# Kernel optimization log

Hardware: AMD Instinct MI355X
Metric: run time of the kernel (lower is better)

Reference implementation:

```python
import jax, jax.numpy as jnp
import numpy as np

B, S, E = 2, 2048, 1024
H, KV, D = 16, 4, 64
GC = 128          # ve_gate_channels
EPS = 1.1920929e-07  # torch F.rms_norm default eps for fp32
NEG = -1e30


def setup_inputs() -> dict:
    key = jax.random.key(0)
    ks = jax.random.split(key, 8)
    x = jax.random.normal(ks[0], (B, S, E), jnp.float32)
    ve = jax.random.normal(ks[1], (B, S, KV * D), jnp.float32)
    half = D // 2
    inv_freq = 1.0 / (10000.0 ** (np.arange(half, dtype=np.float64) / half))
    ang = np.arange(S, dtype=np.float64)[:, None] * inv_freq[None, :]
    cos = jnp.asarray(np.cos(ang), jnp.float32)[:, None, :]  # [S,1,D/2]
    sin = jnp.asarray(np.sin(ang), jnp.float32)[:, None, :]
    sc = E ** -0.5
    Wq = jax.random.normal(ks[2], (E, H * D), jnp.float32) * sc
    Wk = jax.random.normal(ks[3], (E, KV * D), jnp.float32) * sc
    Wv = jax.random.normal(ks[4], (E, KV * D), jnp.float32) * sc
    Wproj = jax.random.normal(ks[5], (E, E), jnp.float32) * sc
    Wgate = jax.random.normal(ks[6], (GC, KV), jnp.float32) * (GC ** -0.5)
    return {"x": x, "ve": ve, "cos": cos, "sin": sin, "Wq": Wq, "Wk": Wk,
            "Wv": Wv, "Wproj": Wproj, "Wgate": Wgate,
            "window_left": 1024, "window_right": 0}


def _rms(x):
    return x * jax.lax.rsqrt(jnp.mean(x * x, axis=-1, keepdims=True) + EPS)


def _rope(x, cos, sin):
    d = x.shape[-1] // 2
    x1, x2 = x[..., :d], x[..., d:]
    return jnp.concatenate([x1 * cos + x2 * sin, -x1 * sin + x2 * cos], axis=-1)


def reference(x, ve, cos, sin, Wq, Wk, Wv, Wproj, Wgate, window_left, window_right):
    b, s, e = x.shape
    q = (x @ Wq).reshape(b, s, H, D)
    k = (x @ Wk).reshape(b, s, KV, D)
    v = (x @ Wv).reshape(b, s, KV, D)
    # value-embedding gate: 2*sigmoid over first GC channels, per kv-head
    gate = 2.0 * jax.nn.sigmoid(x[..., :GC] @ Wgate)          # [B,S,KV]
    v = v + gate[..., None] * ve.reshape(b, s, KV, D)
    q = _rms(_rope(q, cos, sin))
    k = _rms(_rope(k, cos, sin))
    # GQA: repeat kv heads to match query heads
    g = H // KV
    kk = jnp.repeat(k, g, axis=2)                             # [B,S,H,D]
    vv = jnp.repeat(v, g, axis=2)
    scores = jnp.einsum('bihd,bjhd->bhij', q, kk) * (D ** -0.5)
    i = jnp.arange(s)[:, None]
    j = jnp.arange(s)[None, :]
    mask = (j <= i + window_right) & (j >= i - window_left) & (j <= i)
    scores = jnp.where(mask, scores, NEG)
    p = jax.nn.softmax(scores, axis=-1)
    y = jnp.einsum('bhij,bjhd->bihd', p, vv).reshape(b, s, H * D)
    return y @ Wproj
```

## Files before the change

kernel.cpp:

```cpp
#include <hip/hip_runtime.h>

typedef __bf16 bf16;
typedef __bf16 bf16x4 __attribute__((ext_vector_type(4)));
typedef __bf16 bf16x8 __attribute__((ext_vector_type(8)));
typedef float floatx4 __attribute__((ext_vector_type(4)));

#define EPS 1.1920929e-07f
#define QSCALE (0.125f * 1.44269504088896f)
#define SHIFT_C 11.5416f

__device__ __forceinline__ floatx4 mfma16(bf16x8 a, bf16x8 b, floatx4 c) {
  return __builtin_amdgcn_mfma_f32_16x16x32_bf16(a, b, c, 0, 0, 0);
}

__device__ __forceinline__ void gload16(const void* g, void* l) {
  __builtin_amdgcn_global_load_lds((const __attribute__((address_space(1))) unsigned int*)g,
                                   (__attribute__((address_space(3))) unsigned int*)l, 16, 0, 0);
}

__global__ void prep_kernel(const float* __restrict__ x, const float* __restrict__ wgate,
                            const float* __restrict__ Wq, const float* __restrict__ Wk,
                            const float* __restrict__ Wv, const float* __restrict__ Wproj,
                            bf16* __restrict__ xb, float* __restrict__ gate,
                            bf16* __restrict__ out_qkv, bf16* __restrict__ out_proj) {
  __shared__ float tile[32][33];
  const int tid = threadIdx.x;
  if (blockIdx.x < 4096) {
    int t = blockIdx.x;
    const float* xr = x + (size_t)t * 1024;
    float4 v = *(const float4*)(xr + tid * 4);
    bf16x4 o = {(bf16)v.x, (bf16)v.y, (bf16)v.z, (bf16)v.w};
    *(bf16x4*)(xb + (size_t)t * 1024 + tid * 4) = o;
    if (tid < 64) {
      int c = (tid & 31) * 4;
#pragma unroll
      for (int kv = 0; kv < 4; kv++) {
        float g = v.x * wgate[(c + 0) * 4 + kv] + v.y * wgate[(c + 1) * 4 + kv] +
                  v.z * wgate[(c + 2) * 4 + kv] + v.w * wgate[(c + 3) * 4 + kv];
        g += __shfl_xor(g, 1, 64);
        g += __shfl_xor(g, 2, 64);
        g += __shfl_xor(g, 4, 64);
        g += __shfl_xor(g, 8, 64);
        g += __shfl_xor(g, 16, 64);
        if (tid == 0) {
          int b = t >> 11, s = t & 2047;
          gate[((size_t)b * 4 + kv) * 2048 + s] = 2.f / (1.f + __expf(-g));
        }
      }
    }
  } else {
    int j = blockIdx.x - 4096;
    int ky = j / 80;
    int nx = j - ky * 80;
    int k0 = ky * 32;
    int tx = tid & 31, ty = tid >> 5;
    if (nx < 48) {
      int n0 = nx * 32;
#pragma unroll
      for (int i = 0; i < 4; i++) {
        int k = k0 + ty + i * 8, n = n0 + tx;
        float v;
        if (n < 1024)      v = Wq[(size_t)k * 1024 + n];
        else if (n < 1280) v = Wk[(size_t)k * 256 + (n - 1024)];
        else               v = Wv[(size_t)k * 256 + (n - 1280)];
        tile[ty + i * 8][tx] = v;
      }
      __syncthreads();
#pragma unroll
      for (int i = 0; i < 4; i++) {
        int n = n0 + ty + i * 8, k = k0 + tx;
        out_qkv[(size_t)n * 1024 + k] = (bf16)tile[tx][ty + i * 8];
      }
    } else {
      int n0 = (nx - 48) * 32;
#pragma unroll
      for (int i = 0; i < 4; i++)
        tile[ty + i * 8][tx] = Wproj[(size_t)(k0 + ty + i * 8) * 1024 + n0 + tx];
      __syncthreads();
#pragma unroll
      for (int i = 0; i < 4; i++)
        out_proj[(size_t)(n0 + ty + i * 8) * 1024 + k0 + tx] = (bf16)tile[tx][ty + i * 8];
    }
  }
}

__global__ __launch_bounds__(256) void qkv_gemm_kernel(const bf16* __restrict__ A,
                                                       const bf16* __restrict__ Bt,
                                                       const float* __restrict__ ve,
                                                       const float* __restrict__ cosb,
                                                       const float* __restrict__ sinb,
                                                       const float* __restrict__ gate,
                                                       bf16* __restrict__ Qb,
                                                       bf16* __restrict__ Kf,
                                                       bf16* __restrict__ Vf) {
  __shared__ __align__(16) char smem[24576];
  bf16* As = (bf16*)smem;
  bf16* Bs = (bf16*)(smem + 16384);
  bf16* Ep = (bf16*)smem;
  const int K = 1024;
  const int tid = threadIdx.x;
  const int orig = blockIdx.x;
  const int lid = (orig & 7) * 96 + (orig >> 3);
  const int tile = lid % 24;
  const int m0 = (lid / 24) * 128, n0 = tile * 64;
  const int w = tid >> 6, lane = tid & 63;
  const int q = lane >> 4, r0 = lane & 15;
  const int lrow = lane >> 2, lcol = (lane & 3) * 8;
  const int b = m0 >> 11, s0 = m0 & 2047;

  floatx4 acc[2][4];
#pragma unroll
  for (int i = 0; i < 2; i++)
#pragma unroll
    for (int j = 0; j < 4; j++) acc[i][j] = (floatx4){0.f, 0.f, 0.f, 0.f};

  for (int k0 = 0; k0 < K; k0 += 64) {
    __syncthreads();
#pragma unroll
    for (int i = 0; i < 4; i++) {
      int g = w * 4 + i, s = g >> 3, rb = g & 7;
      gload16(A + (size_t)(m0 + rb * 16 + lrow) * K + k0 + s * 32 + lcol, &As[s * 4096 + rb * 512]);
    }
#pragma unroll
    for (int i = 0; i < 2; i++) {
      int g = w * 2 + i, s = g >> 2, rb = g & 3;
      gload16(Bt + (size_t)(n0 + rb * 16 + lrow) * K + k0 + s * 32 + lcol, &Bs[s * 2048 + rb * 512]);
    }
    __syncthreads();
#pragma unroll
    for (int s = 0; s < 2; s++) {
      bf16x8 af[2], bfr[4];
#pragma unroll
      for (int mt = 0; mt < 2; mt++) af[mt] = *(const bf16x8*)&As[s * 4096 + (w * 32 + mt * 16 + r0) * 32 + q * 8];
#pragma unroll
      for (int nt = 0; nt < 4; nt++) bfr[nt] = *(const bf16x8*)&Bs[s * 2048 + (nt * 16 + r0) * 32 + q * 8];
#pragma unroll
      for (int mt = 0; mt < 2; mt++)
#pragma unroll
        for (int nt = 0; nt < 4; nt++)
          acc[mt][nt] = mfma16(af[mt], bfr[nt], acc[mt][nt]);
    }
  }
  __syncthreads();

  if (tile < 16) {
    const int h = tile;
#pragma unroll
    for (int mt = 0; mt < 2; mt++) {
      float rvv[4][4];
#pragma unroll
      for (int ntp = 0; ntp < 2; ntp++) {
        int d31 = ntp * 16 + r0;
#pragma unroll
        for (int r = 0; r < 4; r++) {
          int s = s0 + w * 32 + mt * 16 + q * 4 + r;
          float c = cosb[s * 32 + d31], sn = sinb[s * 32 + d31];
          float v1 = acc[mt][ntp][r], v2 = acc[mt][ntp + 2][r];
          rvv[ntp][r] = v1 * c + v2 * sn;
          rvv[ntp + 2][r] = v2 * c - v1 * sn;
        }
      }
#pragma unroll
      for (int r = 0; r < 4; r++) {
        float ss = 0.f;
#pragma unroll
        for (int nt = 0; nt < 4; nt++) ss += rvv[nt][r] * rvv[nt][r];
        ss += __shfl_xor(ss, 1, 64);
        ss += __shfl_xor(ss, 2, 64);
        ss += __shfl_xor(ss, 4, 64);
        ss += __shfl_xor(ss, 8, 64);
        float sc = rsqrtf(ss * (1.f / 64.f) + EPS) * QSCALE;
        int row = w * 32 + mt * 16 + q * 4 + r;
#pragma unroll
        for (int nt = 0; nt < 4; nt++)
          Ep[row * 72 + nt * 16 + r0] = (bf16)(rvv[nt][r] * sc);
      }
    }
    __syncthreads();
#pragma unroll
    for (int p = 0; p < 4; p++) {
      int g = p * 256 + tid;
      int row = g >> 3, chunk = g & 7;
      *(uint4*)&Qb[(((size_t)b * 16 + h) * 2048 + s0 + row) * 64 + chunk * 8] =
          *(const uint4*)&Ep[row * 72 + chunk * 8];
    }
  } else if (tile < 20) {
    const int kv = tile - 16;
#pragma unroll
    for (int mt = 0; mt < 2; mt++) {
      float rvv[4][4];
#pragma unroll
      for (int ntp = 0; ntp < 2; ntp++) {
        int d31 = ntp * 16 + r0;
#pragma unroll
        for (int r = 0; r < 4; r++) {
          int s = s0 + w * 32 + mt * 16 + q * 4 + r;
          float c = cosb[s * 32 + d31], sn = sinb[s * 32 + d31];
          float v1 = acc[mt][ntp][r], v2 = acc[mt][ntp + 2][r];
          rvv[ntp][r] = v1 * c + v2 * sn;
          rvv[ntp + 2][r] = v2 * c - v1 * sn;
        }
      }
#pragma unroll
      for (int r = 0; r < 4; r++) {
        float ss = 0.f;
#pragma unroll
        for (int nt = 0; nt < 4; nt++) ss += rvv[nt][r] * rvv[nt][r];
        ss += __shfl_xor(ss, 1, 64);
        ss += __shfl_xor(ss, 2, 64);
        ss += __shfl_xor(ss, 4, 64);
        ss += __shfl_xor(ss, 8, 64);
        float sc = rsqrtf(ss * (1.f / 64.f) + EPS);
        int row = w * 32 + mt * 16 + q * 4 + r;
#pragma unroll
        for (int nt = 0; nt < 4; nt++)
          Ep[row * 72 + nt * 16 + r0] = (bf16)(rvv[nt][r] * sc);
      }
    }
    __syncthreads();
    {
      int tk = (s0 >> 5) + w;
      size_t tb = ((size_t)(b * 4 + kv) * 64 + tk) * 2048;
#pragma unroll
      for (int u = 0; u < 4; u++) {
        int joff = (u >= 2) ? 16 : 0, doff = (u & 1) * 32;
        bf16x8 f = *(const bf16x8*)&Ep[(w * 32 + joff + r0) * 72 + doff + q * 8];
        *(bf16x8*)&Kf[tb + u * 512 + lane * 8] = f;
      }
    }
  } else {
    const int kv = tile - 20;
    const float* gbase = gate + ((size_t)b * 4 + kv) * 2048;
#pragma unroll
    for (int mt = 0; mt < 2; mt++) {
#pragma unroll
      for (int r = 0; r < 4; r++) {
        int row = w * 32 + mt * 16 + q * 4 + r;
        float gg = gbase[s0 + row];
#pragma unroll
        for (int nt = 0; nt < 4; nt++) {
          int d = nt * 16 + r0;
          float vv = acc[mt][nt][r] + gg * ve[(size_t)(m0 + row) * 256 + kv * 64 + d];
          Ep[row * 72 + d] = (bf16)vv;
        }
      }
    }
    __syncthreads();
    {
      int tk = (s0 >> 5) + w;
      size_t tb = ((size_t)(b * 4 + kv) * 64 + tk) * 2048;
#pragma unroll
      for (int nt = 0; nt < 4; nt++) {
        bf16 tmp[8];
#pragma unroll
        for (int e = 0; e < 8; e++) {
          int jl = w * 32 + (e >> 2) * 16 + 4 * q + (e & 3);
          tmp[e] = Ep[jl * 72 + nt * 16 + r0];
        }
        *(uint4*)&Vf[tb + nt * 512 + lane * 8] = *(uint4*)tmp;
      }
    }
  }
}

__global__ __launch_bounds__(256) void proj_gemm_kernel(const bf16* __restrict__ A,
                                                        const bf16* __restrict__ Bt,
                                                        float* __restrict__ Cout) {
  __shared__ __align__(16) bf16 As[2 * 128 * 32];
  __shared__ __align__(16) bf16 Bs[2 * 64 * 32];
  const int K = 1024, N = 1024;
  const int tid = threadIdx.x;
  const int orig = blockIdx.x;
  const int lid = (orig & 7) * 64 + (orig >> 3);
  const int m0 = (lid / 16) * 128, n0 = (lid % 16) * 64;
  const int w = tid >> 6, lane = tid & 63;
  const int q = lane >> 4, r0 = lane & 15;
  const int lrow = lane >> 2, lcol = (lane & 3) * 8;

  floatx4 acc[2][4];
#pragma unroll
  for (int i = 0; i < 2; i++)
#pragma unroll
    for (int j = 0; j < 4; j++) acc[i][j] = (floatx4){0.f, 0.f, 0.f, 0.f};

  for (int k0 = 0; k0 < K; k0 += 64) {
    __syncthreads();
#pragma unroll
    for (int i = 0; i < 4; i++) {
      int g = w * 4 + i, s = g >> 3, rb = g & 7;
      gload16(A + (size_t)(m0 + rb * 16 + lrow) * K + k0 + s * 32 + lcol, &As[s * 4096 + rb * 512]);
    }
#pragma unroll
    for (int i = 0; i < 2; i++) {
      int g = w * 2 + i, s = g >> 2, rb = g & 3;
      gload16(Bt + (size_t)(n0 + rb * 16 + lrow) * K + k0 + s * 32 + lcol, &Bs[s * 2048 + rb * 512]);
    }
    __syncthreads();
#pragma unroll
    for (int s = 0; s < 2; s++) {
      bf16x8 af[2], bfr[4];
#pragma unroll
      for (int mt = 0; mt < 2; mt++) af[mt] = *(const bf16x8*)&As[s * 4096 + (w * 32 + mt * 16 + r0) * 32 + q * 8];
#pragma unroll
      for (int nt = 0; nt < 4; nt++) bfr[nt] = *(const bf16x8*)&Bs[s * 2048 + (nt * 16 + r0) * 32 + q * 8];
#pragma unroll
      for (int mt = 0; mt < 2; mt++)
#pragma unroll
        for (int nt = 0; nt < 4; nt++)
          acc[mt][nt] = mfma16(af[mt], bfr[nt], acc[mt][nt]);
    }
  }
#pragma unroll
  for (int mt = 0; mt < 2; mt++)
#pragma unroll
    for (int nt = 0; nt < 4; nt++)
#pragma unroll
      for (int r = 0; r < 4; r++) {
        int row = m0 + w * 32 + mt * 16 + q * 4 + r;
        int col = n0 + nt * 16 + r0;
        Cout[(size_t)row * N + col] = acc[mt][nt][r];
      }
}

__global__ __launch_bounds__(256, 4) void attn_kernel(const bf16* __restrict__ Qb,
                                                      const bf16* __restrict__ Kf,
                                                      const bf16* __restrict__ Vf,
                                                      const int* __restrict__ wlp,
                                                      const int* __restrict__ wrp,
                                                      bf16* __restrict__ Yb) {
  const int wl = wlp[0];
  const int wrc = min(wrp[0], 0);
  const int blk = blockIdx.x;
  const int bkv = blk & 7;
  const int b = bkv >> 2, kvh = bkv & 3;
  const int cm = 127 - (blk >> 3);
  const int w = threadIdx.x >> 6, lane = threadIdx.x & 63;
  const int q = lane >> 4, r0 = lane & 15;
  const int h = kvh * 4 + w;
  const int q0 = cm << 4;

  const bf16* qbase = Qb + (((size_t)b * 16 + h) * 2048 + q0 + r0) * 64;
  bf16x8 aq0 = *(const bf16x8*)(qbase + q * 8);
  bf16x8 aq1 = *(const bf16x8*)(qbase + 32 + q * 8);

  floatx4 O[4];
#pragma unroll
  for (int nt = 0; nt < 4; nt++) O[nt] = (floatx4){0.f, 0.f, 0.f, 0.f};
  floatx4 L = (floatx4){0.f, 0.f, 0.f, 0.f};

  const bf16 onev = (bf16)1.0f;
  const bf16x8 ones = {onev, onev, onev, onev, onev, onev, onev, onev};

  const int jlo = max(0, q0 - wl) & ~31;
  const int jhi = q0 + 15 + wrc;
  const int count = ((jhi - jlo) >> 5) + 1;
  const int tile0 = jlo >> 5;

  const bf16* kfb = Kf + ((size_t)(b * 4 + kvh) * 64) * 2048 + lane * 8;
  const bf16* vfb = Vf + ((size_t)(b * 4 + kvh) * 64) * 2048 + lane * 8;

  bf16x8 kf[4], nk[4], vf[4];
#pragma unroll
  for (int u = 0; u < 4; u++)
    kf[u] = *(const bf16x8*)(kfb + (size_t)tile0 * 2048 + u * 512);

  for (int t = 0; t < count; t++) {
    const int j0 = jlo + (t << 5);
    const int tcur = tile0 + t;
    const int tn = (t + 1 < count) ? tcur + 1 : tcur;
#pragma unroll
    for (int u = 0; u < 4; u++) nk[u] = *(const bf16x8*)(kfb + (size_t)tn * 2048 + u * 512);
#pragma unroll
    for (int u = 0; u < 4; u++) vf[u] = *(const bf16x8*)(vfb + (size_t)tcur * 2048 + u * 512);

    floatx4 s0 = (floatx4){-SHIFT_C, -SHIFT_C, -SHIFT_C, -SHIFT_C};
    floatx4 s1 = s0;
    __builtin_amdgcn_s_setprio(1);
    s0 = mfma16(kf[0], aq0, s0);
    s0 = mfma16(kf[1], aq1, s0);
    s1 = mfma16(kf[2], aq0, s1);
    s1 = mfma16(kf[3], aq1, s1);
    __builtin_amdgcn_s_setprio(0);

    bf16x8 pa;
    if (j0 >= q0 + 15 - wl && j0 + 31 <= q0 + wrc) {
#pragma unroll
      for (int r = 0; r < 4; r++) {
        pa[r] = (bf16)exp2f(s0[r]);
        pa[4 + r] = (bf16)exp2f(s1[r]);
      }
    } else {
      const int i = q0 + r0;
#pragma unroll
      for (int r = 0; r < 4; r++) {
        int ja = j0 + 4 * q + r, jb = ja + 16;
        bool va = (ja <= i + wrc) && (ja >= i - wl);
        bool vb = (jb <= i + wrc) && (jb >= i - wl);
        pa[r] = va ? (bf16)exp2f(s0[r]) : (bf16)0.f;
        pa[4 + r] = vb ? (bf16)exp2f(s1[r]) : (bf16)0.f;
      }
    }

    __builtin_amdgcn_s_setprio(1);
    L = mfma16(pa, ones, L);
#pragma unroll
    for (int nt = 0; nt < 4; nt++) O[nt] = mfma16(pa, vf[nt], O[nt]);
    __builtin_amdgcn_s_setprio(0);

#pragma unroll
    for (int u = 0; u < 4; u++) kf[u] = nk[u];
  }

  float inv[4];
#pragma unroll
  for (int r = 0; r < 4; r++) inv[r] = 1.f / L[r];
#pragma unroll
  for (int nt = 0; nt < 4; nt++)
#pragma unroll
    for (int r = 0; r < 4; r++) {
      int i = q0 + q * 4 + r;
      Yb[((size_t)b * 2048 + i) * 1024 + h * 64 + nt * 16 + r0] = (bf16)(O[nt][r] * inv[r]);
    }
}

extern "C" void kernel_launch(void* const* d_in, const int* in_sizes, int n_in,
                              void* d_out, int out_size, void* d_ws, size_t ws_size,
                              hipStream_t stream) {
  const float* x     = (const float*)d_in[0];
  const float* ve    = (const float*)d_in[1];
  const float* cosb  = (const float*)d_in[2];
  const float* sinb  = (const float*)d_in[3];
  const float* Wq    = (const float*)d_in[4];
  const float* Wk    = (const float*)d_in[5];
  const float* Wv    = (const float*)d_in[6];
  const float* Wproj = (const float*)d_in[7];
  const float* Wgate = (const float*)d_in[8];
  const int* wl      = (const int*)d_in[9];
  const int* wr      = (const int*)d_in[10];

  char* ws = (char*)d_ws;
  bf16* Xb      = (bf16*)(ws);
  bf16* Wqkv_t  = (bf16*)(ws + 8388608);
  bf16* Wproj_t = (bf16*)(ws + 11534336);
  bf16* Qb      = (bf16*)(ws + 13631488);
  bf16* Kf      = (bf16*)(ws + 22020096);
  bf16* Vf      = (bf16*)(ws + 24117248);
  bf16* Yb      = (bf16*)(ws + 26214400);
  float* gateb  = (float*)(ws + 34603008);

  prep_kernel<<<4096 + 2560, 256, 0, stream>>>(x, Wgate, Wq, Wk, Wv, Wproj, Xb, gateb, Wqkv_t, Wproj_t);
  qkv_gemm_kernel<<<768, 256, 0, stream>>>(Xb, Wqkv_t, ve, cosb, sinb, gateb, Qb, Kf, Vf);
  attn_kernel<<<1024, 256, 0, stream>>>(Qb, Kf, Vf, wl, wr, Yb);
  proj_gemm_kernel<<<512, 256, 0, stream>>>(Yb, Wproj_t, (float*)d_out);
}
```

Before: 166.1 us.

## Stage K/V tiles in shared memory via direct global-to-LDS loads per block

Each of the four waves (one per query head sharing a KV head) previously loaded the full K and V tile into registers from global memory on its own, with K prefetched one tile ahead. Now the block loads each K/V tile once into LDS with global_load_lds, split across the waves, and every wave reads its fragments from LDS. This cuts redundant global/L2 traffic by a factor of four. In exchange it adds two __syncthreads per tile and drops the register prefetch, so the load latency is no longer overlapped with compute.

```diff
diff --git a/kernel.cpp b/kernel.cpp
--- a/kernel.cpp
+++ b/kernel.cpp
@@ -328,6 +328,8 @@
                                                       const int* __restrict__ wlp,
                                                       const int* __restrict__ wrp,
                                                       bf16* __restrict__ Yb) {
+  __shared__ __align__(16) bf16 Ks[2048];
+  __shared__ __align__(16) bf16 Vs[2048];
   const int wl = wlp[0];
   const int wrc = min(wrp[0], 0);
   const int blk = blockIdx.x;
@@ -356,30 +358,34 @@
   const int count = ((jhi - jlo) >> 5) + 1;
   const int tile0 = jlo >> 5;
 
-  const bf16* kfb = Kf + ((size_t)(b * 4 + kvh) * 64) * 2048 + lane * 8;
-  const bf16* vfb = Vf + ((size_t)(b * 4 + kvh) * 64) * 2048 + lane * 8;
-
-  bf16x8 kf[4], nk[4], vf[4];
-#pragma unroll
-  for (int u = 0; u < 4; u++)
-    kf[u] = *(const bf16x8*)(kfb + (size_t)tile0 * 2048 + u * 512);
+  const bf16* kfb = Kf + ((size_t)(b * 4 + kvh) * 64) * 2048;
+  const bf16* vfb = Vf + ((size_t)(b * 4 + kvh) * 64) * 2048;
 
   for (int t = 0; t < count; t++) {
     const int j0 = jlo + (t << 5);
-    const int tcur = tile0 + t;
-    const int tn = (t + 1 < count) ? tcur + 1 : tcur;
-#pragma unroll
-    for (int u = 0; u < 4; u++) nk[u] = *(const bf16x8*)(kfb + (size_t)tn * 2048 + u * 512);
-#pragma unroll
-    for (int u = 0; u < 4; u++) vf[u] = *(const bf16x8*)(vfb + (size_t)tcur * 2048 + u * 512);
+    const bf16* kt = kfb + (size_t)(tile0 + t) * 2048;
+    const bf16* vt = vfb + (size_t)(tile0 + t) * 2048;
+    __syncthreads();
+#pragma unroll
+    for (int i = 0; i < 2; i++) {
+      int c = 2 * w + i;
+      if (c < 4) gload16(kt + c * 512 + lane * 8, &Ks[c * 512]);
+      else       gload16(vt + (c - 4) * 512 + lane * 8, &Vs[(c - 4) * 512]);
+    }
+    __syncthreads();
+
+    bf16x8 kf0 = *(const bf16x8*)&Ks[0 * 512 + lane * 8];
+    bf16x8 kf1 = *(const bf16x8*)&Ks[1 * 512 + lane * 8];
+    bf16x8 kf2 = *(const bf16x8*)&Ks[2 * 512 + lane * 8];
+    bf16x8 kf3 = *(const bf16x8*)&Ks[3 * 512 + lane * 8];
 
     floatx4 s0 = (floatx4){-SHIFT_C, -SHIFT_C, -SHIFT_C, -SHIFT_C};
     floatx4 s1 = s0;
     __builtin_amdgcn_s_setprio(1);
-    s0 = mfma16(kf[0], aq0, s0);
-    s0 = mfma16(kf[1], aq1, s0);
-    s1 = mfma16(kf[2], aq0, s1);
-    s1 = mfma16(kf[3], aq1, s1);
+    s0 = mfma16(kf0, aq0, s0);
+    s0 = mfma16(kf1, aq1, s0);
+    s1 = mfma16(kf2, aq0, s1);
+    s1 = mfma16(kf3, aq1, s1);
     __builtin_amdgcn_s_setprio(0);
 
     bf16x8 pa;
@@ -401,14 +407,18 @@
       }
     }
 
+    bf16x8 vf0 = *(const bf16x8*)&Vs[0 * 512 + lane * 8];
+    bf16x8 vf1 = *(const bf16x8*)&Vs[1 * 512 + lane * 8];
+    bf16x8 vf2 = *(const bf16x8*)&Vs[2 * 512 + lane * 8];
+    bf16x8 vf3 = *(const bf16x8*)&Vs[3 * 512 + lane * 8];
+
     __builtin_amdgcn_s_setprio(1);
     L = mfma16(pa, ones, L);
-#pragma unroll
-    for (int nt = 0; nt < 4; nt++) O[nt] = mfma16(pa, vf[nt], O[nt]);
+    O[0] = mfma16(pa, vf0, O[0]);
+    O[1] = mfma16(pa, vf1, O[1]);
+    O[2] = mfma16(pa, vf2, O[2]);
+    O[3] = mfma16(pa, vf3, O[3]);
     __builtin_amdgcn_s_setprio(0);
-
-#pragma unroll
-    for (int u = 0; u < 4; u++) kf[u] = nk[u];
   }
 
   float inv[4];
```

New measurement: 163.3 us. About the same (-1.6%).
